# Optimization experiments

Measured on AMD Instinct MI355X. Metric: run time of the kernel, lower is better.

## Reference

```python
import jax, jax.numpy as jnp
import numpy as np

MODES = (16, 16, 16)  # (kx, ky, kz); rfft keeps kz//2+1 = 9 modes on last axis


def setup_inputs() -> dict:
    key = jax.random.key(0)
    k_x, k_w1, k_w2 = jax.random.split(key, 3)
    B, C, H, W, D = 4, 64, 64, 64, 64
    hidden = C // 4
    kzr = MODES[2] // 2 + 1
    gate_dim = MODES[0] * MODES[1] * kzr  # 16*16*9 = 2304
    x = jax.random.normal(k_x, (B, C, H, W, D), dtype=jnp.float32)
    w1 = jax.random.normal(k_w1, (C, hidden), dtype=jnp.float32) * (1.0 / np.sqrt(C))
    b1 = jnp.zeros((hidden,), dtype=jnp.float32)
    w2 = jax.random.normal(k_w2, (hidden, gate_dim), dtype=jnp.float32) * (1.0 / np.sqrt(hidden))
    b2 = jnp.zeros((gate_dim,), dtype=jnp.float32)
    return {"x": x, "w1": w1, "b1": b1, "w2": w2, "b2": b2}


def reference(x, w1, b1, w2, b2):
    B = x.shape[0]
    kx, ky, kz = MODES
    kzr = kz // 2 + 1
    # Gate network: global average pool over spatial dims -> MLP -> sigmoid
    pooled = jnp.mean(x, axis=(2, 3, 4))                      # [B, C]
    h = jax.nn.relu(pooled @ w1 + b1)                          # [B, C//4]
    gates = jax.nn.sigmoid(h @ w2 + b2)                        # [B, kx*ky*kzr]
    gates = gates.reshape(B, 1, kx, ky, kzr)                   # broadcast over channels
    # Full 3D rFFT, gate only the low-frequency corner block, inverse FFT
    x_ft = jnp.fft.rfftn(x, axes=(-3, -2, -1))                 # [B, C, H, W, D//2+1] complex
    x_ft_gated = x_ft.at[:, :, :kx, :ky, :kzr].multiply(gates.astype(x_ft.real.dtype))
    out = jnp.fft.irfftn(x_ft_gated, s=x.shape[-3:], axes=(-3, -2, -1))
    return out.astype(x.dtype)
```

## Files before the change

kernel.cpp:

```cpp
#include <hip/hip_runtime.h>

namespace {

constexpr float COS64[64] = {
  1.00000000f,  0.99518473f,  0.98078528f,  0.95694034f,
  0.92387953f,  0.88192126f,  0.83146961f,  0.77301045f,
  0.70710678f,  0.63439328f,  0.55557023f,  0.47139674f,
  0.38268343f,  0.29028468f,  0.19509032f,  0.09801714f,
  0.00000000f, -0.09801714f, -0.19509032f, -0.29028468f,
 -0.38268343f, -0.47139674f, -0.55557023f, -0.63439328f,
 -0.70710678f, -0.77301045f, -0.83146961f, -0.88192126f,
 -0.92387953f, -0.95694034f, -0.98078528f, -0.99518473f,
 -1.00000000f, -0.99518473f, -0.98078528f, -0.95694034f,
 -0.92387953f, -0.88192126f, -0.83146961f, -0.77301045f,
 -0.70710678f, -0.63439328f, -0.55557023f, -0.47139674f,
 -0.38268343f, -0.29028468f, -0.19509032f, -0.09801714f,
 -0.00000000f,  0.09801714f,  0.19509032f,  0.29028468f,
  0.38268343f,  0.47139674f,  0.55557023f,  0.63439328f,
  0.70710678f,  0.77301045f,  0.83146961f,  0.88192126f,
  0.92387953f,  0.95694034f,  0.98078528f,  0.99518473f };

constexpr float TWOPI_64 = 0.09817477042468103f;
constexpr int MM = 144;
constexpr int GD = 2304;

__device__ __forceinline__ void rot_mi(int m, float r_in, float i_in,
                                       float& r_out, float& i_out) {
  float r  = (m & 1) ? i_in : r_in;
  float i2 = (m & 1) ? r_in : i_in;
  r  = (m >= 2) ? -r : r;
  i2 = (m == 1 || m == 2) ? -i2 : i2;
  r_out = r; i_out = i2;
}

__global__ __launch_bounds__(256) void k1_fwd(const float* __restrict__ x,
                                              float2* __restrict__ buf1) {
  __shared__ float xs[64 * 68];
  __shared__ float2 As[9 * 67];
  const int tid = threadIdx.x;
  const int slice = blockIdx.x;
  const int w = tid >> 2, q = tid & 3;

  const float4* xp = (const float4*)(x + ((size_t)slice << 12));
  const float4 a0 = xp[tid];
  const float4 a1 = xp[tid + 256];
  const float4 a2 = xp[tid + 512];
  const float4 a3 = xp[tid + 768];
  {
    const int s0 = tid & 15, hi = tid >> 4;
    *(float4*)&xs[(hi +  0) * 68 + s0 * 4] = a0;
    *(float4*)&xs[(hi + 16) * 68 + s0 * 4] = a1;
    *(float4*)&xs[(hi + 32) * 68 + s0 * 4] = a2;
    *(float4*)&xs[(hi + 48) * 68 + s0 * 4] = a3;
  }
  __syncthreads();

  float xv[16];
  {
    const float4 b0 = *(const float4*)&xs[w * 68 + q * 16 + 0];
    const float4 b1 = *(const float4*)&xs[w * 68 + q * 16 + 4];
    const float4 b2 = *(const float4*)&xs[w * 68 + q * 16 + 8];
    const float4 b3 = *(const float4*)&xs[w * 68 + q * 16 + 12];
    xv[0]=b0.x; xv[1]=b0.y; xv[2]=b0.z; xv[3]=b0.w;
    xv[4]=b1.x; xv[5]=b1.y; xv[6]=b1.z; xv[7]=b1.w;
    xv[8]=b2.x; xv[9]=b2.y; xv[10]=b2.z; xv[11]=b2.w;
    xv[12]=b3.x; xv[13]=b3.y; xv[14]=b3.z; xv[15]=b3.w;
  }

  float ar[9], ai[9];
#pragma unroll
  for (int kz = 0; kz < 9; ++kz) { ar[kz] = 0.f; ai[kz] = 0.f; }
#pragma unroll
  for (int j = 0; j < 16; ++j) {
    const float v = xv[j];
#pragma unroll
    for (int kz = 0; kz < 9; ++kz) {
      const int n = (kz * j) & 63;
      ar[kz] = fmaf(v, COS64[n], ar[kz]);
      ai[kz] = fmaf(v, -COS64[(n + 48) & 63], ai[kz]);
    }
  }
#pragma unroll
  for (int kz = 0; kz < 9; ++kz) {
    const int m = (q * kz) & 3;
    float r, i2;
    rot_mi(m, ar[kz], ai[kz], r, i2);
    r  += __shfl_xor(r, 1);  r  += __shfl_xor(r, 2);
    i2 += __shfl_xor(i2, 1); i2 += __shfl_xor(i2, 2);
    if (q == 0) As[kz * 67 + w] = make_float2(r, i2);
  }
  __syncthreads();

  if (tid < MM) {
    const int ky = tid / 9, kz = tid - ky * 9;
    const float cs = COS64[ky], sn = COS64[(ky + 48) & 63];
    const int m1 = ky & 3, m2 = (2 * ky) & 3, m3 = (3 * ky) & 3;
    float px = 1.f, py = 0.f, br = 0.f, bi = 0.f;
    const float2* Ak = As + kz * 67;
#pragma unroll
    for (int b = 0; b < 16; ++b) {
      const float2 v0 = Ak[b];
      const float2 v1 = Ak[b + 16];
      const float2 v2 = Ak[b + 32];
      const float2 v3 = Ak[b + 48];
      float gr = v0.x, gi = v0.y, rr, ri;
      rot_mi(m1, v1.x, v1.y, rr, ri); gr += rr; gi += ri;
      rot_mi(m2, v2.x, v2.y, rr, ri); gr += rr; gi += ri;
      rot_mi(m3, v3.x, v3.y, rr, ri); gr += rr; gi += ri;
      br = fmaf(gr, px, fmaf(-gi, py, br));
      bi = fmaf(gr, py, fmaf( gi, px, bi));
      const float nx = fmaf(px, cs,  py * sn);
      const float ny = fmaf(py, cs, -px * sn);
      px = nx; py = ny;
    }
    buf1[(size_t)slice * MM + tid] = make_float2(br, bi);
  }
}

__global__ __launch_bounds__(256) void k2_fwd(const float2* __restrict__ buf1,
                                              float2* __restrict__ buf2) {
  __shared__ float2 Bs[32 * MM];
  const int tid = threadIdx.x, bc = blockIdx.x;
  const int kx = tid >> 4, g = tid & 15;

  float accR[9], accI[9];
#pragma unroll
  for (int j = 0; j < 9; ++j) { accR[j] = 0.f; accI[j] = 0.f; }
  float qR = 1.f, qI = 0.f;
  const float hc = COS64[kx], hsn = COS64[(kx + 48) & 63];

  const float4* src = (const float4*)(buf1 + (size_t)bc * 64 * MM);
  for (int c2 = 0; c2 < 2; ++c2) {
    float4* dst4 = (float4*)Bs;
    for (int i = tid; i < 2304; i += 256) dst4[i] = src[c2 * 2304 + i];
    __syncthreads();
    for (int hh = 0; hh < 32; ++hh) {
      const float2* row = Bs + hh * MM + g * 9;
#pragma unroll
      for (int j = 0; j < 9; ++j) {
        const float2 b = row[j];
        accR[j] = fmaf(b.x, qR, fmaf(-b.y, qI, accR[j]));
        accI[j] = fmaf(b.x, qI, fmaf( b.y, qR, accI[j]));
      }
      const float nR = fmaf(qR, hc, qI * hsn);
      const float nI = fmaf(qI, hc, -qR * hsn);
      qR = nR; qI = nI;
    }
    __syncthreads();
  }

  float2* dst = buf2 + (size_t)bc * GD + kx * MM + g * 9;
#pragma unroll
  for (int j = 0; j < 9; ++j) dst[j] = make_float2(accR[j], accI[j]);
}

__global__ __launch_bounds__(256) void k3_gates(const float2* __restrict__ buf2,
    const float* __restrict__ w1, const float* __restrict__ b1,
    const float* __restrict__ w2, const float* __restrict__ b2,
    float* __restrict__ gm1) {
  __shared__ float pooled[64];
  __shared__ float hs[16];
  const int b = blockIdx.x, tid = threadIdx.x;
  if (tid < 64)
    pooled[tid] = buf2[(size_t)(b * 64 + tid) * GD].x * (1.f / 262144.f);
  __syncthreads();
  if (tid < 16) {
    float acc = b1[tid];
    for (int c = 0; c < 64; ++c) acc = fmaf(pooled[c], w1[c * 16 + tid], acc);
    hs[tid] = fmaxf(acc, 0.f);
  }
  __syncthreads();
#pragma unroll
  for (int r = 0; r < 9; ++r) {
    const int o = tid + r * 256;
    float acc = b2[o];
#pragma unroll
    for (int j = 0; j < 16; ++j) acc = fmaf(hs[j], w2[j * GD + o], acc);
    gm1[b * GD + o] = 1.f / (1.f + expf(-acc)) - 1.f;
  }
}

__global__ __launch_bounds__(256) void k4a_c1(const float2* __restrict__ S,
                                              const float* __restrict__ gm1,
                                              float2* __restrict__ C1buf) {
  __shared__ float2 Dg[GD];
  __shared__ float2 rotS[64 * 16];
  const int tid = threadIdx.x, bc = blockIdx.x, b = bc >> 6;

  for (int i = tid; i < GD; i += 256) {
    const float2 sv = S[(size_t)bc * GD + i];
    const float g = gm1[(size_t)b * GD + i];
    Dg[i] = make_float2(sv.x * g, sv.y * g);
  }
#pragma unroll
  for (int u = 0; u < 4; ++u) {
    const int e = tid * 4 + u, hh = e >> 4, kx = e & 15;
    const int n = (kx * hh) & 63;
    rotS[e] = make_float2(COS64[n], COS64[(n + 48) & 63]);
  }
  __syncthreads();

  const int h = tid >> 2, mq = tid & 3;
  float2* dst = C1buf + ((size_t)(bc * 64 + h)) * MM + mq * 36;
  for (int jb = 0; jb < 3; ++jb) {
    float aR[12], aI[12];
#pragma unroll
    for (int j = 0; j < 12; ++j) { aR[j] = 0.f; aI[j] = 0.f; }
    for (int kx = 0; kx < 16; ++kx) {
      const float2 rot = rotS[h * 16 + kx];
      const float2* drow = Dg + kx * MM + mq * 36 + jb * 12;
#pragma unroll
      for (int j = 0; j < 12; ++j) {
        const float2 d = drow[j];
        aR[j] = fmaf(d.x, rot.x, fmaf(-d.y, rot.y, aR[j]));
        aI[j] = fmaf(d.x, rot.y, fmaf( d.y, rot.x, aI[j]));
      }
    }
#pragma unroll
    for (int j = 0; j < 12; ++j) dst[jb * 12 + j] = make_float2(aR[j], aI[j]);
  }
}

__global__ __launch_bounds__(256) void k4b_final(const float2* __restrict__ C1buf,
                                                 const float* __restrict__ x,
                                                 float* __restrict__ out) {
  __shared__ float2 C1s[MM];
  __shared__ float2 C2s[9 * 65];
  __shared__ float deltaS[64 * 68];
  const int tid = threadIdx.x;
  const int slice = 16383 - blockIdx.x;
  const int w = tid >> 2, q = tid & 3;

  const float4* xp = (const float4*)(x + ((size_t)slice << 12));
  const float4 xv0 = xp[tid];
  const float4 xv1 = xp[tid + 256];
  const float4 xv2 = xp[tid + 512];
  const float4 xv3 = xp[tid + 768];

  if (tid < 72) {
    const float4* cp = (const float4*)(C1buf + (size_t)slice * MM);
    ((float4*)C1s)[tid] = cp[tid];
  }
  __syncthreads();

  {
    float sn, cs;
    sincosf(TWOPI_64 * (float)w, &sn, &cs);
    const int kz0 = q, kz1 = q + 4;
    float a0r = 0.f, a0i = 0.f, a1r = 0.f, a1i = 0.f, a2r = 0.f, a2i = 0.f;
    float px = 1.f, py = 0.f;
    for (int ky = 0; ky < 16; ++ky) {
      const float2 c0 = C1s[ky * 9 + kz0];
      const float2 c1 = C1s[ky * 9 + kz1];
      a0r = fmaf(c0.x, px, fmaf(-c0.y, py, a0r));
      a0i = fmaf(c0.x, py, fmaf( c0.y, px, a0i));
      a1r = fmaf(c1.x, px, fmaf(-c1.y, py, a1r));
      a1i = fmaf(c1.x, py, fmaf( c1.y, px, a1i));
      if (q == 0) {
        const float2 c2v = C1s[ky * 9 + 8];
        a2r = fmaf(c2v.x, px, fmaf(-c2v.y, py, a2r));
        a2i = fmaf(c2v.x, py, fmaf( c2v.y, px, a2i));
      }
      const float nx = fmaf(px, cs, -py * sn);
      const float ny = fmaf(px, sn,  py * cs);
      px = nx; py = ny;
    }
    C2s[kz0 * 65 + w] = make_float2(a0r, a0i);
    C2s[kz1 * 65 + w] = make_float2(a1r, a1i);
    if (q == 0) C2s[8 * 65 + w] = make_float2(a2r, a2i);
  }
  __syncthreads();

  {
    float cr[9], ci[9];
#pragma unroll
    for (int kz = 0; kz < 9; ++kz) {
      const float2 v = C2s[kz * 65 + w];
      const int m = (kz * q) & 3;
      const float a = v.x, b2_ = v.y;
      float r  = (m & 1) ? b2_ : a;
      float i2 = (m & 1) ? a : b2_;
      r  = (m == 1 || m == 2) ? -r : r;
      i2 = (m >= 2) ? -i2 : i2;
      cr[kz] = r; ci[kz] = i2;
    }
    float acc[16];
#pragma unroll
    for (int j = 0; j < 16; ++j) acc[j] = cr[0];
#pragma unroll
    for (int kz = 1; kz < 9; ++kz) {
#pragma unroll
      for (int j = 0; j < 16; ++j) {
        const int n = (kz * j) & 63;
        acc[j] = fmaf(cr[kz],  2.f * COS64[n], acc[j]);
        acc[j] = fmaf(ci[kz], -2.f * COS64[(n + 48) & 63], acc[j]);
      }
    }
    const float scale = 1.f / 262144.f;
    float4 d0, d1, d2, d3;
    d0.x = acc[0]  * scale; d0.y = acc[1]  * scale;
    d0.z = acc[2]  * scale; d0.w = acc[3]  * scale;
    d1.x = acc[4]  * scale; d1.y = acc[5]  * scale;
    d1.z = acc[6]  * scale; d1.w = acc[7]  * scale;
    d2.x = acc[8]  * scale; d2.y = acc[9]  * scale;
    d2.z = acc[10] * scale; d2.w = acc[11] * scale;
    d3.x = acc[12] * scale; d3.y = acc[13] * scale;
    d3.z = acc[14] * scale; d3.w = acc[15] * scale;
    *(float4*)&deltaS[w * 68 + q * 16 + 0]  = d0;
    *(float4*)&deltaS[w * 68 + q * 16 + 4]  = d1;
    *(float4*)&deltaS[w * 68 + q * 16 + 8]  = d2;
    *(float4*)&deltaS[w * 68 + q * 16 + 12] = d3;
  }
  __syncthreads();

  {
    const int s0 = tid & 15, hi = tid >> 4;
    const float4 r0 = *(const float4*)&deltaS[(hi +  0) * 68 + s0 * 4];
    const float4 r1 = *(const float4*)&deltaS[(hi + 16) * 68 + s0 * 4];
    const float4 r2 = *(const float4*)&deltaS[(hi + 32) * 68 + s0 * 4];
    const float4 r3 = *(const float4*)&deltaS[(hi + 48) * 68 + s0 * 4];
    float4* op = (float4*)(out + ((size_t)slice << 12));
    float4 o0 = xv0, o1 = xv1, o2 = xv2, o3 = xv3;
    o0.x += r0.x; o0.y += r0.y; o0.z += r0.z; o0.w += r0.w;
    o1.x += r1.x; o1.y += r1.y; o1.z += r1.z; o1.w += r1.w;
    o2.x += r2.x; o2.y += r2.y; o2.z += r2.z; o2.w += r2.w;
    o3.x += r3.x; o3.y += r3.y; o3.z += r3.z; o3.w += r3.w;
    op[tid]       = o0;
    op[tid + 256] = o1;
    op[tid + 512] = o2;
    op[tid + 768] = o3;
  }
}

}

extern "C" void kernel_launch(void* const* d_in, const int* in_sizes, int n_in,
                              void* d_out, int out_size, void* d_ws, size_t ws_size,
                              hipStream_t stream) {
  (void)in_sizes; (void)n_in; (void)out_size; (void)ws_size;
  const float* x  = (const float*)d_in[0];
  const float* w1 = (const float*)d_in[1];
  const float* b1 = (const float*)d_in[2];
  const float* w2 = (const float*)d_in[3];
  const float* b2 = (const float*)d_in[4];
  float* out = (float*)d_out;

  char* ws = (char*)d_ws;
  float2* buf1  = (float2*)ws;
  float2* buf2  = (float2*)(ws + 18874368);
  float*  gm1   = (float*)(ws + 23592960);
  float2* c1buf = (float2*)(ws + 23629824);

  hipLaunchKernelGGL(k1_fwd,   dim3(16384),    dim3(256), 0, stream, x, buf1);
  hipLaunchKernelGGL(k2_fwd,   dim3(256),      dim3(256), 0, stream, buf1, buf2);
  hipLaunchKernelGGL(k3_gates, dim3(4),        dim3(256), 0, stream, buf2, w1, b1, w2, b2, gm1);
  hipLaunchKernelGGL(k4a_c1,   dim3(256),      dim3(256), 0, stream, buf2, gm1, c1buf);
  hipLaunchKernelGGL(k4b_final,dim3(16384),    dim3(256), 0, stream, c1buf, x, out);
}
```

Measured before the change: 234.6 us.

## Fuse k2 forward transform with gated inverse stage; streamline final kernel

```diff
diff --git a/kernel.cpp b/kernel.cpp
--- a/kernel.cpp
+++ b/kernel.cpp
@@ -20,7 +20,6 @@
   0.70710678f,  0.77301045f,  0.83146961f,  0.88192126f,
   0.92387953f,  0.95694034f,  0.98078528f,  0.99518473f };
 
-constexpr float TWOPI_64 = 0.09817477042468103f;
 constexpr int MM = 144;
 constexpr int GD = 2304;
 
@@ -117,11 +116,53 @@
   }
 }
 
+__global__ __launch_bounds__(256) void k3_gates(const float2* __restrict__ buf1,
+    const float* __restrict__ w1, const float* __restrict__ b1,
+    const float* __restrict__ w2, const float* __restrict__ b2,
+    float* __restrict__ gm1) {
+  __shared__ float pooled[64];
+  __shared__ float hs[16];
+  const int b = blockIdx.x, tid = threadIdx.x;
+  const int c = tid >> 2, q = tid & 3;
+  {
+    const float2* bp = buf1 + ((size_t)((b * 64 + c) * 64) + q) * MM;
+    float s = 0.f;
+    for (int t = 0; t < 16; ++t) s += bp[(size_t)t * 4 * MM].x;
+    s += __shfl_xor(s, 1); s += __shfl_xor(s, 2);
+    if (q == 0) pooled[c] = s * (1.f / 262144.f);
+  }
+  __syncthreads();
+  if (tid < 16) {
+    float acc = b1[tid];
+    for (int cc = 0; cc < 64; ++cc) acc = fmaf(pooled[cc], w1[cc * 16 + tid], acc);
+    hs[tid] = fmaxf(acc, 0.f);
+  }
+  __syncthreads();
+#pragma unroll
+  for (int r = 0; r < 9; ++r) {
+    const int o = tid + r * 256;
+    float acc = b2[o];
+#pragma unroll
+    for (int j = 0; j < 16; ++j) acc = fmaf(hs[j], w2[j * GD + o], acc);
+    gm1[b * GD + o] = 1.f / (1.f + expf(-acc)) - 1.f;
+  }
+}
+
 __global__ __launch_bounds__(256) void k2_fwd(const float2* __restrict__ buf1,
-                                              float2* __restrict__ buf2) {
+                                              const float* __restrict__ gm1,
+                                              float2* __restrict__ C1buf) {
   __shared__ float2 Bs[32 * MM];
-  const int tid = threadIdx.x, bc = blockIdx.x;
+  __shared__ float2 Dg[GD];
+  __shared__ float2 rotS[64 * 16];
+  const int tid = threadIdx.x, bc = blockIdx.x, b = bc >> 6;
   const int kx = tid >> 4, g = tid & 15;
+
+#pragma unroll
+  for (int u = 0; u < 4; ++u) {
+    const int e = tid * 4 + u, hh = e >> 4, kxx = e & 15;
+    const int n = (kxx * hh) & 63;
+    rotS[e] = make_float2(COS64[n], COS64[(n + 48) & 63]);
+  }
 
   float accR[9], accI[9];
 #pragma unroll
@@ -138,9 +179,9 @@
       const float2* row = Bs + hh * MM + g * 9;
 #pragma unroll
       for (int j = 0; j < 9; ++j) {
-        const float2 b = row[j];
-        accR[j] = fmaf(b.x, qR, fmaf(-b.y, qI, accR[j]));
-        accI[j] = fmaf(b.x, qI, fmaf( b.y, qR, accI[j]));
+        const float2 bv = row[j];
+        accR[j] = fmaf(bv.x, qR, fmaf(-bv.y, qI, accR[j]));
+        accI[j] = fmaf(bv.x, qI, fmaf( bv.y, qR, accI[j]));
       }
       const float nR = fmaf(qR, hc, qI * hsn);
       const float nI = fmaf(qI, hc, -qR * hsn);
@@ -149,75 +190,37 @@
     __syncthreads();
   }
 
-  float2* dst = buf2 + (size_t)bc * GD + kx * MM + g * 9;
-#pragma unroll
-  for (int j = 0; j < 9; ++j) dst[j] = make_float2(accR[j], accI[j]);
-}
-
-__global__ __launch_bounds__(256) void k3_gates(const float2* __restrict__ buf2,
-    const float* __restrict__ w1, const float* __restrict__ b1,
-    const float* __restrict__ w2, const float* __restrict__ b2,
-    float* __restrict__ gm1) {
-  __shared__ float pooled[64];
-  __shared__ float hs[16];
-  const int b = blockIdx.x, tid = threadIdx.x;
-  if (tid < 64)
-    pooled[tid] = buf2[(size_t)(b * 64 + tid) * GD].x * (1.f / 262144.f);
-  __syncthreads();
-  if (tid < 16) {
-    float acc = b1[tid];
-    for (int c = 0; c < 64; ++c) acc = fmaf(pooled[c], w1[c * 16 + tid], acc);
-    hs[tid] = fmaxf(acc, 0.f);
-  }
-  __syncthreads();
-#pragma unroll
-  for (int r = 0; r < 9; ++r) {
-    const int o = tid + r * 256;
-    float acc = b2[o];
-#pragma unroll
-    for (int j = 0; j < 16; ++j) acc = fmaf(hs[j], w2[j * GD + o], acc);
-    gm1[b * GD + o] = 1.f / (1.f + expf(-acc)) - 1.f;
-  }
-}
-
-__global__ __launch_bounds__(256) void k4a_c1(const float2* __restrict__ S,
-                                              const float* __restrict__ gm1,
-                                              float2* __restrict__ C1buf) {
-  __shared__ float2 Dg[GD];
-  __shared__ float2 rotS[64 * 16];
-  const int tid = threadIdx.x, bc = blockIdx.x, b = bc >> 6;
-
-  for (int i = tid; i < GD; i += 256) {
-    const float2 sv = S[(size_t)bc * GD + i];
-    const float g = gm1[(size_t)b * GD + i];
-    Dg[i] = make_float2(sv.x * g, sv.y * g);
-  }
-#pragma unroll
-  for (int u = 0; u < 4; ++u) {
-    const int e = tid * 4 + u, hh = e >> 4, kx = e & 15;
-    const int n = (kx * hh) & 63;
-    rotS[e] = make_float2(COS64[n], COS64[(n + 48) & 63]);
-  }
-  __syncthreads();
-
-  const int h = tid >> 2, mq = tid & 3;
-  float2* dst = C1buf + ((size_t)(bc * 64 + h)) * MM + mq * 36;
-  for (int jb = 0; jb < 3; ++jb) {
-    float aR[12], aI[12];
-#pragma unroll
-    for (int j = 0; j < 12; ++j) { aR[j] = 0.f; aI[j] = 0.f; }
-    for (int kx = 0; kx < 16; ++kx) {
-      const float2 rot = rotS[h * 16 + kx];
-      const float2* drow = Dg + kx * MM + mq * 36 + jb * 12;
-#pragma unroll
-      for (int j = 0; j < 12; ++j) {
-        const float2 d = drow[j];
-        aR[j] = fmaf(d.x, rot.x, fmaf(-d.y, rot.y, aR[j]));
-        aI[j] = fmaf(d.x, rot.y, fmaf( d.y, rot.x, aI[j]));
+  {
+    const float* gp = gm1 + (size_t)b * GD + kx * MM + g * 9;
+    float2* dp = Dg + kx * MM + g * 9;
+#pragma unroll
+    for (int j = 0; j < 9; ++j) {
+      const float gg = gp[j];
+      dp[j] = make_float2(accR[j] * gg, accI[j] * gg);
+    }
+  }
+  __syncthreads();
+
+  {
+    const int h = tid >> 2, mq = tid & 3;
+    float2* dst = C1buf + ((size_t)(bc * 64 + h)) * MM + mq * 36;
+    for (int jb = 0; jb < 3; ++jb) {
+      float aR[12], aI[12];
+#pragma unroll
+      for (int j = 0; j < 12; ++j) { aR[j] = 0.f; aI[j] = 0.f; }
+      for (int kxx = 0; kxx < 16; ++kxx) {
+        const float2 rot = rotS[h * 16 + kxx];
+        const float2* drow = Dg + kxx * MM + mq * 36 + jb * 12;
+#pragma unroll
+        for (int j = 0; j < 12; ++j) {
+          const float2 d = drow[j];
+          aR[j] = fmaf(d.x, rot.x, fmaf(-d.y, rot.y, aR[j]));
+          aI[j] = fmaf(d.x, rot.y, fmaf( d.y, rot.x, aI[j]));
+        }
       }
-    }
-#pragma unroll
-    for (int j = 0; j < 12; ++j) dst[jb * 12 + j] = make_float2(aR[j], aI[j]);
+#pragma unroll
+      for (int j = 0; j < 12; ++j) dst[jb * 12 + j] = make_float2(aR[j], aI[j]);
+    }
   }
 }
 
@@ -226,10 +229,10 @@
                                                  float* __restrict__ out) {
   __shared__ float2 C1s[MM];
   __shared__ float2 C2s[9 * 65];
-  __shared__ float deltaS[64 * 68];
   const int tid = threadIdx.x;
   const int slice = 16383 - blockIdx.x;
   const int w = tid >> 2, q = tid & 3;
+  const int s0 = tid & 15, hi = tid >> 4;
 
   const float4* xp = (const float4*)(x + ((size_t)slice << 12));
   const float4 xv0 = xp[tid];
@@ -244,8 +247,7 @@
   __syncthreads();
 
   {
-    float sn, cs;
-    sincosf(TWOPI_64 * (float)w, &sn, &cs);
+    const float cs = COS64[w], sn = COS64[(w + 48) & 63];
     const int kz0 = q, kz1 = q + 4;
     float a0r = 0.f, a0i = 0.f, a1r = 0.f, a1i = 0.f, a2r = 0.f, a2i = 0.f;
     float px = 1.f, py = 0.f;
@@ -265,70 +267,47 @@
       const float ny = fmaf(px, sn,  py * cs);
       px = nx; py = ny;
     }
-    C2s[kz0 * 65 + w] = make_float2(a0r, a0i);
-    C2s[kz1 * 65 + w] = make_float2(a1r, a1i);
-    if (q == 0) C2s[8 * 65 + w] = make_float2(a2r, a2i);
-  }
-  __syncthreads();
-
-  {
-    float cr[9], ci[9];
+    const float scale = 1.f / 262144.f;
+    C2s[kz0 * 65 + w] = make_float2(a0r * scale, a0i * scale);
+    C2s[kz1 * 65 + w] = make_float2(a1r * scale, a1i * scale);
+    if (q == 0) C2s[8 * 65 + w] = make_float2(a2r * scale, a2i * scale);
+  }
+  __syncthreads();
+
+  {
+    float phR[9], phI[9];
 #pragma unroll
     for (int kz = 0; kz < 9; ++kz) {
-      const float2 v = C2s[kz * 65 + w];
-      const int m = (kz * q) & 3;
-      const float a = v.x, b2_ = v.y;
-      float r  = (m & 1) ? b2_ : a;
-      float i2 = (m & 1) ? a : b2_;
-      r  = (m == 1 || m == 2) ? -r : r;
-      i2 = (m >= 2) ? -i2 : i2;
-      cr[kz] = r; ci[kz] = i2;
-    }
-    float acc[16];
-#pragma unroll
-    for (int j = 0; j < 16; ++j) acc[j] = cr[0];
-#pragma unroll
-    for (int kz = 1; kz < 9; ++kz) {
-#pragma unroll
-      for (int j = 0; j < 16; ++j) {
-        const int n = (kz * j) & 63;
-        acc[j] = fmaf(cr[kz],  2.f * COS64[n], acc[j]);
-        acc[j] = fmaf(ci[kz], -2.f * COS64[(n + 48) & 63], acc[j]);
+      const int n = (4 * s0 * kz) & 63;
+      phR[kz] = COS64[n];
+      phI[kz] = COS64[(n + 48) & 63];
+    }
+    float4* op = (float4*)(out + ((size_t)slice << 12));
+#pragma unroll
+    for (int k = 0; k < 4; ++k) {
+      const int wk = hi + 16 * k;
+      const float4 xv = (k == 0) ? xv0 : (k == 1) ? xv1 : (k == 2) ? xv2 : xv3;
+      const float2 c0 = C2s[0 * 65 + wk];
+      float o[4];
+#pragma unroll
+      for (int j = 0; j < 4; ++j) o[j] = c0.x;
+#pragma unroll
+      for (int kz = 1; kz < 9; ++kz) {
+        const float2 c = C2s[kz * 65 + wk];
+        const float cr = c.x * phR[kz] - c.y * phI[kz];
+        const float ci = c.x * phI[kz] + c.y * phR[kz];
+#pragma unroll
+        for (int j = 0; j < 4; ++j) {
+          const int n = (kz * j) & 63;
+          o[j] = fmaf(cr,  2.f * COS64[n], o[j]);
+          o[j] = fmaf(ci, -2.f * COS64[(n + 48) & 63], o[j]);
+        }
       }
-    }
-    const float scale = 1.f / 262144.f;
-    float4 d0, d1, d2, d3;
-    d0.x = acc[0]  * scale; d0.y = acc[1]  * scale;
-    d0.z = acc[2]  * scale; d0.w = acc[3]  * scale;
-    d1.x = acc[4]  * scale; d1.y = acc[5]  * scale;
-    d1.z = acc[6]  * scale; d1.w = acc[7]  * scale;
-    d2.x = acc[8]  * scale; d2.y = acc[9]  * scale;
-    d2.z = acc[10] * scale; d2.w = acc[11] * scale;
-    d3.x = acc[12] * scale; d3.y = acc[13] * scale;
-    d3.z = acc[14] * scale; d3.w = acc[15] * scale;
-    *(float4*)&deltaS[w * 68 + q * 16 + 0]  = d0;
-    *(float4*)&deltaS[w * 68 + q * 16 + 4]  = d1;
-    *(float4*)&deltaS[w * 68 + q * 16 + 8]  = d2;
-    *(float4*)&deltaS[w * 68 + q * 16 + 12] = d3;
-  }
-  __syncthreads();
-
-  {
-    const int s0 = tid & 15, hi = tid >> 4;
-    const float4 r0 = *(const float4*)&deltaS[(hi +  0) * 68 + s0 * 4];
-    const float4 r1 = *(const float4*)&deltaS[(hi + 16) * 68 + s0 * 4];
-    const float4 r2 = *(const float4*)&deltaS[(hi + 32) * 68 + s0 * 4];
-    const float4 r3 = *(const float4*)&deltaS[(hi + 48) * 68 + s0 * 4];
-    float4* op = (float4*)(out + ((size_t)slice << 12));
-    float4 o0 = xv0, o1 = xv1, o2 = xv2, o3 = xv3;
-    o0.x += r0.x; o0.y += r0.y; o0.z += r0.z; o0.w += r0.w;
-    o1.x += r1.x; o1.y += r1.y; o1.z += r1.z; o1.w += r1.w;
-    o2.x += r2.x; o2.y += r2.y; o2.z += r2.z; o2.w += r2.w;
-    o3.x += r3.x; o3.y += r3.y; o3.z += r3.z; o3.w += r3.w;
-    op[tid]       = o0;
-    op[tid + 256] = o1;
-    op[tid + 512] = o2;
-    op[tid + 768] = o3;
+      float4 ov;
+      ov.x = xv.x + o[0]; ov.y = xv.y + o[1];
+      ov.z = xv.z + o[2]; ov.w = xv.w + o[3];
+      op[tid + 256 * k] = ov;
+    }
   }
 }
 
@@ -347,13 +326,11 @@
 
   char* ws = (char*)d_ws;
   float2* buf1  = (float2*)ws;
-  float2* buf2  = (float2*)(ws + 18874368);
-  float*  gm1   = (float*)(ws + 23592960);
-  float2* c1buf = (float2*)(ws + 23629824);
+  float*  gm1   = (float*)(ws + 18874368);
+  float2* c1buf = (float2*)(ws + 18911232);
 
   hipLaunchKernelGGL(k1_fwd,   dim3(16384),    dim3(256), 0, stream, x, buf1);
-  hipLaunchKernelGGL(k2_fwd,   dim3(256),      dim3(256), 0, stream, buf1, buf2);
-  hipLaunchKernelGGL(k3_gates, dim3(4),        dim3(256), 0, stream, buf2, w1, b1, w2, b2, gm1);
-  hipLaunchKernelGGL(k4a_c1,   dim3(256),      dim3(256), 0, stream, buf2, gm1, c1buf);
+  hipLaunchKernelGGL(k3_gates, dim3(4),        dim3(256), 0, stream, buf1, w1, b1, w2, b2, gm1);
+  hipLaunchKernelGGL(k2_fwd,   dim3(256),      dim3(256), 0, stream, buf1, gm1, c1buf);
   hipLaunchKernelGGL(k4b_final,dim3(16384),    dim3(256), 0, stream, c1buf, x, out);
 }
```

After: 255.5 us. +8.9%, slower.
